# Optimization experiments

Measured on AMD Instinct MI355X. Metric: run time of the kernel, lower is better.

The kernel has to match this reference:

```python
import jax, jax.numpy as jnp
import numpy as np

L, S, N, E = 1024, 1024, 16, 1024

def setup_inputs() -> dict:
    key = jax.random.key(0)
    ks = jax.random.split(key, 7)
    return {
        "query": jax.random.normal(ks[0], (L, N, E), dtype=jnp.float32),
        "key": jax.random.normal(ks[1], (S, N, E), dtype=jnp.float32),
        "value": jax.random.normal(ks[2], (S, N, E), dtype=jnp.float32),
        "q_proj_weight": jax.random.normal(ks[3], (E, E), dtype=jnp.float32) * (E ** -0.5),
        "k_proj_weight": jax.random.normal(ks[4], (E, E), dtype=jnp.float32) * (E ** -0.5),
        "v_proj_weight": jax.random.normal(ks[5], (E, E), dtype=jnp.float32) * (E ** -0.5),
        "in_proj_bias": jax.random.normal(ks[6], (3 * E,), dtype=jnp.float32) * 0.02,
    }

def reference(query, key, value, q_proj_weight, k_proj_weight, v_proj_weight, in_proj_bias):
    # query: (L, N, E); key/value: (S, N, E); single head => head_dim = E
    e = query.shape[-1]
    scaling = jnp.asarray(e, query.dtype) ** -0.5
    # F.linear(x, W, b) = x @ W.T + b
    q = (jnp.einsum("lne,fe->lnf", query, q_proj_weight) + in_proj_bias[:e]) * scaling
    k = jnp.einsum("sne,fe->snf", key, k_proj_weight) + in_proj_bias[e:2 * e]
    v = jnp.einsum("sne,fe->snf", value, v_proj_weight) + in_proj_bias[2 * e:]
    # scores: (N, L, S)
    scores = jnp.einsum("lne,sne->nls", q, k)
    attn = jax.nn.softmax(scores, axis=-1)
    # output back to (L, N, E)
    out = jnp.einsum("nls,sne->lne", attn, v)
    return out
```

## Files before the change

kernel.cpp:

```cpp
#include <hip/hip_runtime.h>
#include <stdint.h>


typedef __attribute__((ext_vector_type(8))) short bf16x8;
typedef __attribute__((ext_vector_type(4))) float f32x4;

__device__ __forceinline__ float bf2f(unsigned short u) {
    union { unsigned int i; float f; } w; w.i = ((unsigned int)u) << 16; return w.f;
}
__device__ __forceinline__ unsigned short f2bf(float f) {
    union { float f; unsigned int i; } w; w.f = f;
    unsigned int r = (w.i + 0x7FFFu + ((w.i >> 16) & 1u)) >> 16;
    return (unsigned short)r;
}

__device__ __forceinline__ void g2l16(const unsigned short* g, unsigned short* l) {
    __builtin_amdgcn_global_load_lds(
        (const __attribute__((address_space(1))) unsigned int*)g,
        (__attribute__((address_space(3))) unsigned int*)l, 16, 0, 0);
}

#define BM 256
#define BN 256
#define BK 32

template <int BIAS_MODE, typename OutT>
__global__ __launch_bounds__(1024, 4) void gemm_bt2(
    const unsigned short* __restrict__ A,
    const unsigned short* __restrict__ B,
    OutT* __restrict__ C,
    const float* __restrict__ bias,
    float scale, int K,
    long lda, long ldb, long ldc,
    long aBatch, long bBatch, long cBatch,
    int gridM, int gridN)
{
    __shared__ __align__(16) unsigned short lds[65536];

    const int tid  = threadIdx.x;
    const int wave = tid >> 6;
    const int lane = tid & 63;
    const int lr   = lane & 15;
    const int q4   = lane >> 4;
    const int wm   = wave >> 2;
    const int wn   = wave & 3;

    const int p    = blockIdx.x;
    const int l    = ((p & 7) << 5) + (p >> 3);
    const int bcol = l % gridN;
    const int t2   = l / gridN;
    const int brow = t2 % gridM;
    const int bz   = t2 / gridM;

    const long m0 = (long)brow * BM;
    const long n0 = (long)bcol * BN;
    A += (long)bz * aBatch;
    B += (long)bz * bBatch;
    C += (long)bz * cBatch;

    const int tswz  = tid ^ ((tid >> 3) & 7);
    const int srow  = tswz >> 2;
    const int skoff = (tswz & 3) * 8;
    const unsigned short* aS = A + (m0 + srow) * lda + skoff;
    const unsigned short* bS = B + (n0 + srow) * ldb + skoff;
    const int ldsW = wave * 512;

    const int myoff = (((lr << 2) | q4) ^ ((lr >> 1) & 7)) << 3;

    f32x4 acc[4][4];
    const f32x4 zero = {0.f, 0.f, 0.f, 0.f};
#pragma unroll
    for (int m = 0; m < 4; m++)
#pragma unroll
        for (int n = 0; n < 4; n++) acc[m][n] = zero;

    const int nkt = K / BK;

#pragma unroll
    for (int t = 0; t < 3; t++) {
        const long kb = (long)t * BK;
        unsigned short* base = &lds[t * 16384];
        g2l16(aS + kb, base + ldsW);
        g2l16(bS + kb, base + 8192 + ldsW);
    }
    asm volatile("s_waitcnt vmcnt(4)" ::: "memory");
    __builtin_amdgcn_sched_barrier(0);
    __builtin_amdgcn_s_barrier();

    for (int kt = 0; kt < nkt; kt++) {
        const int buf  = kt & 3;
        const int sbuf = (kt + 3) & 3;
        const int st   = (kt + 3 < nkt) ? kt + 3 : nkt - 1;
        const long kb  = (long)st * BK;
        const unsigned short* At = &lds[buf * 16384];
        const unsigned short* Bt = At + 8192;
        unsigned short* sb = &lds[sbuf * 16384];

        g2l16(aS + kb, sb + ldsW);
        g2l16(bS + kb, sb + 8192 + ldsW);

        bf16x8 af[4], bfr[4];
#pragma unroll
        for (int m = 0; m < 4; m++)
            af[m] = *(const bf16x8*)&At[(wm * 64 + m * 16) * 32 + myoff];
#pragma unroll
        for (int n = 0; n < 4; n++)
            bfr[n] = *(const bf16x8*)&Bt[(wn * 64 + n * 16) * 32 + myoff];

        __builtin_amdgcn_s_setprio(1);
#pragma unroll
        for (int m = 0; m < 4; m++)
#pragma unroll
            for (int n = 0; n < 4; n++)
                acc[m][n] = __builtin_amdgcn_mfma_f32_16x16x32_bf16(
                    af[m], bfr[n], acc[m][n], 0, 0, 0);
        __builtin_amdgcn_s_setprio(0);

        asm volatile("s_waitcnt vmcnt(4)" ::: "memory");
        __builtin_amdgcn_sched_barrier(0);
        __builtin_amdgcn_s_barrier();
    }

    asm volatile("s_waitcnt vmcnt(0)" ::: "memory");
    __syncthreads();

    if constexpr (sizeof(OutT) == 2) {
#pragma unroll
        for (int m = 0; m < 4; m++)
#pragma unroll
            for (int n = 0; n < 4; n++) {
                const int col = wn * 64 + n * 16 + lr;
#pragma unroll
                for (int r = 0; r < 4; r++) {
                    const int row = wm * 64 + m * 16 + q4 * 4 + r;
                    float v = acc[m][n][r];
                    if constexpr (BIAS_MODE == 1) v += bias[n0 + col];
                    if constexpr (BIAS_MODE == 2) v += bias[m0 + row];
                    v *= scale;
                    lds[row * 256 + (col ^ (((row >> 2) & 3) << 4))] = f2bf(v);
                }
            }
        __syncthreads();
#pragma unroll
        for (int i = 0; i < 8; i++) {
            const int g   = i * 1024 + tid;
            const int row = g >> 5;
            const int ch  = g & 31;
            bf16x8 v = *(const bf16x8*)&lds[row * 256 + ((ch * 8) ^ (((row >> 2) & 3) << 4))];
            *(bf16x8*)((unsigned short*)C + (m0 + row) * ldc + n0 + ch * 8) = v;
        }
    } else {
        float* fl = (float*)lds;
#pragma unroll
        for (int h = 0; h < 2; h++) {
            __syncthreads();
            if ((wm >> 1) == h) {
#pragma unroll
                for (int m = 0; m < 4; m++)
#pragma unroll
                    for (int n = 0; n < 4; n++) {
                        const int col = wn * 64 + n * 16 + lr;
#pragma unroll
                        for (int r = 0; r < 4; r++) {
                            const int rowh = (wm & 1) * 64 + m * 16 + q4 * 4 + r;
                            float v = acc[m][n][r];
                            if constexpr (BIAS_MODE == 1) v += bias[n0 + col];
                            if constexpr (BIAS_MODE == 2) v += bias[m0 + h * 128 + rowh];
                            v *= scale;
                            fl[rowh * 256 + (col ^ (((rowh >> 2) & 3) << 4))] = v;
                        }
                    }
            }
            __syncthreads();
#pragma unroll
            for (int i = 0; i < 8; i++) {
                const int g   = i * 1024 + tid;
                const int row = g >> 6;
                const int ch  = g & 63;
                float4 v = *(const float4*)&fl[row * 256 + ((ch * 4) ^ (((row >> 2) & 3) << 4))];
                *(float4*)((float*)C + (m0 + h * 128 + row) * ldc + n0 + ch * 4) = v;
            }
        }
    }
}

__global__ __launch_bounds__(256) void cvt_all(
    const float* __restrict__ q,  unsigned short* __restrict__ qb,
    const float* __restrict__ k,  unsigned short* __restrict__ kb,
    const float* __restrict__ wq, const float* __restrict__ wk,
    const float* __restrict__ wv, unsigned short* __restrict__ wb)
{
    const int b = blockIdx.x;
    const float* src;
    unsigned short* dst;
    long item;
    if (b < 8192)       { src = q; dst = qb; item = (long)b * 256 + threadIdx.x; }
    else if (b < 16384) { src = k; dst = kb; item = (long)(b - 8192) * 256 + threadIdx.x; }
    else {
        const int wsel = (b - 16384) >> 9;
        src = (wsel == 0) ? wq : ((wsel == 1) ? wk : wv);
        dst = wb + (long)wsel * 1048576;
        item = (long)((b - 16384) & 511) * 256 + threadIdx.x;
    }
    const float4* pp = (const float4*)(src + item * 8);
    float4 a = pp[0], c = pp[1];
    bf16x8 v;
    v[0] = (short)f2bf(a.x); v[1] = (short)f2bf(a.y);
    v[2] = (short)f2bf(a.z); v[3] = (short)f2bf(a.w);
    v[4] = (short)f2bf(c.x); v[5] = (short)f2bf(c.y);
    v[6] = (short)f2bf(c.z); v[7] = (short)f2bf(c.w);
    *(bf16x8*)(dst + item * 8) = v;
}

__global__ __launch_bounds__(256) void cvt_one(
    const float* __restrict__ in, unsigned short* __restrict__ out)
{
    const long item = (long)blockIdx.x * 256 + threadIdx.x;
    const float4* pp = (const float4*)(in + item * 8);
    float4 a = pp[0], c = pp[1];
    bf16x8 v;
    v[0] = (short)f2bf(a.x); v[1] = (short)f2bf(a.y);
    v[2] = (short)f2bf(a.z); v[3] = (short)f2bf(a.w);
    v[4] = (short)f2bf(c.x); v[5] = (short)f2bf(c.y);
    v[6] = (short)f2bf(c.z); v[7] = (short)f2bf(c.w);
    *(bf16x8*)(out + item * 8) = v;
}

__global__ __launch_bounds__(256) void softmax_wave(unsigned short* __restrict__ base)
{
    const int wave = threadIdx.x >> 6, lane = threadIdx.x & 63;
    unsigned short* p = base + ((long)blockIdx.x * 4 + wave) * 1024;

    bf16x8 v0 = *(const bf16x8*)(p + lane * 8);
    bf16x8 v1 = *(const bf16x8*)(p + 512 + lane * 8);
    float x[16];
#pragma unroll
    for (int i = 0; i < 8; i++) {
        x[i]     = fminf(fmaxf(bf2f((unsigned short)v0[i]), -1e30f), 1e30f);
        x[8 + i] = fminf(fmaxf(bf2f((unsigned short)v1[i]), -1e30f), 1e30f);
    }
    float m = x[0];
#pragma unroll
    for (int i = 1; i < 16; i++) m = fmaxf(m, x[i]);
#pragma unroll
    for (int o = 32; o > 0; o >>= 1) m = fmaxf(m, __shfl_xor(m, o));

    float e[16], s = 0.f;
#pragma unroll
    for (int i = 0; i < 16; i++) { e[i] = __expf(x[i] - m); s += e[i]; }
#pragma unroll
    for (int o = 32; o > 0; o >>= 1) s += __shfl_xor(s, o);
    const float inv = 1.0f / s;

    bf16x8 o0, o1;
#pragma unroll
    for (int i = 0; i < 8; i++) {
        o0[i] = (short)f2bf(e[i] * inv);
        o1[i] = (short)f2bf(e[8 + i] * inv);
    }
    *(bf16x8*)(p + lane * 8) = o0;
    *(bf16x8*)(p + 512 + lane * 8) = o1;
}

extern "C" void kernel_launch(void* const* d_in, const int* in_sizes, int n_in,
                              void* d_out, int out_size, void* d_ws, size_t ws_size,
                              hipStream_t stream) {
    const float* query = (const float*)d_in[0];
    const float* keyp  = (const float*)d_in[1];
    const float* valp  = (const float*)d_in[2];
    const float* wq    = (const float*)d_in[3];
    const float* wk    = (const float*)d_in[4];
    const float* wv    = (const float*)d_in[5];
    const float* bias  = (const float*)d_in[6];
    float* out = (float*)d_out;

    unsigned short* WSA = (unsigned short*)d_ws;
    unsigned short* WSB = WSA + 16777216;
    unsigned short* OC  = (unsigned short*)d_out;
    unsigned short* OD  = OC + 16777216;

    const dim3 cblk(256, 1, 1);
    const dim3 gblk(1024, 1, 1);

    cvt_all<<<17920, cblk, 0, stream>>>(query, WSA, keyp, WSB, wq, wk, wv, OD);
    gemm_bt2<1, unsigned short><<<256, gblk, 0, stream>>>(
        WSA, OD, OC, bias, 0.03125f, 1024,
        1024, 1024, 1024, 0, 0, 0, 64, 4);
    gemm_bt2<1, unsigned short><<<256, gblk, 0, stream>>>(
        WSB, OD + 1048576, WSA, bias + 1024, 1.0f, 1024,
        1024, 1024, 1024, 0, 0, 0, 64, 4);
    gemm_bt2<0, unsigned short><<<256, gblk, 0, stream>>>(
        OC, WSA, WSB, nullptr, 1.0f, 1024,
        16384, 16384, 1024, 1024, 1024, 1048576, 4, 4);
    softmax_wave<<<4096, cblk, 0, stream>>>(WSB);
    cvt_one<<<8192, cblk, 0, stream>>>(valp, OC);
    gemm_bt2<2, unsigned short><<<256, gblk, 0, stream>>>(
        OD + 2097152, OC, WSA, bias + 2048, 1.0f, 1024,
        1024, 16384, 1024, 0, 1024, 1048576, 4, 4);
    gemm_bt2<0, float><<<256, gblk, 0, stream>>>(
        WSB, WSA, out, nullptr, 1.0f, 1024,
        1024, 1024, 16384, 1048576, 1048576, 1024, 4, 4);
}
```

Measured before the change: 422.5 us.

## Fuse fp32-to-bf16 input conversion into projection GEMM loads

```diff
diff --git a/kernel.cpp b/kernel.cpp
--- a/kernel.cpp
+++ b/kernel.cpp
@@ -24,10 +24,20 @@
 #define BN 256
 #define BK 32
 
-template <int BIAS_MODE, typename OutT>
+#define CVT8(dst8, r0, r1)                                                     \
+    {                                                                          \
+        bf16x8 _v;                                                             \
+        _v[0] = (short)f2bf((r0).x); _v[1] = (short)f2bf((r0).y);              \
+        _v[2] = (short)f2bf((r0).z); _v[3] = (short)f2bf((r0).w);              \
+        _v[4] = (short)f2bf((r1).x); _v[5] = (short)f2bf((r1).y);              \
+        _v[6] = (short)f2bf((r1).z); _v[7] = (short)f2bf((r1).w);              \
+        *(bf16x8*)(dst8) = _v;                                                 \
+    }
+
+template <int BIAS_MODE, typename OutT, bool INF32>
 __global__ __launch_bounds__(1024, 4) void gemm_bt2(
-    const unsigned short* __restrict__ A,
-    const unsigned short* __restrict__ B,
+    const void* __restrict__ Av,
+    const void* __restrict__ Bv,
     OutT* __restrict__ C,
     const float* __restrict__ bias,
     float scale, int K,
@@ -54,16 +64,10 @@
 
     const long m0 = (long)brow * BM;
     const long n0 = (long)bcol * BN;
-    A += (long)bz * aBatch;
-    B += (long)bz * bBatch;
-    C += (long)bz * cBatch;
 
     const int tswz  = tid ^ ((tid >> 3) & 7);
     const int srow  = tswz >> 2;
     const int skoff = (tswz & 3) * 8;
-    const unsigned short* aS = A + (m0 + srow) * lda + skoff;
-    const unsigned short* bS = B + (n0 + srow) * ldb + skoff;
-    const int ldsW = wave * 512;
 
     const int myoff = (((lr << 2) | q4) ^ ((lr >> 1) & 7)) << 3;
 
@@ -76,52 +80,121 @@
 
     const int nkt = K / BK;
 
-#pragma unroll
-    for (int t = 0; t < 3; t++) {
-        const long kb = (long)t * BK;
-        unsigned short* base = &lds[t * 16384];
-        g2l16(aS + kb, base + ldsW);
-        g2l16(bS + kb, base + 8192 + ldsW);
-    }
-    asm volatile("s_waitcnt vmcnt(4)" ::: "memory");
-    __builtin_amdgcn_sched_barrier(0);
-    __builtin_amdgcn_s_barrier();
-
-    for (int kt = 0; kt < nkt; kt++) {
-        const int buf  = kt & 3;
-        const int sbuf = (kt + 3) & 3;
-        const int st   = (kt + 3 < nkt) ? kt + 3 : nkt - 1;
-        const long kb  = (long)st * BK;
-        const unsigned short* At = &lds[buf * 16384];
-        const unsigned short* Bt = At + 8192;
-        unsigned short* sb = &lds[sbuf * 16384];
-
-        g2l16(aS + kb, sb + ldsW);
-        g2l16(bS + kb, sb + 8192 + ldsW);
-
-        bf16x8 af[4], bfr[4];
-#pragma unroll
-        for (int m = 0; m < 4; m++)
-            af[m] = *(const bf16x8*)&At[(wm * 64 + m * 16) * 32 + myoff];
-#pragma unroll
-        for (int n = 0; n < 4; n++)
-            bfr[n] = *(const bf16x8*)&Bt[(wn * 64 + n * 16) * 32 + myoff];
-
-        __builtin_amdgcn_s_setprio(1);
-#pragma unroll
-        for (int m = 0; m < 4; m++)
-#pragma unroll
-            for (int n = 0; n < 4; n++)
-                acc[m][n] = __builtin_amdgcn_mfma_f32_16x16x32_bf16(
-                    af[m], bfr[n], acc[m][n], 0, 0, 0);
-        __builtin_amdgcn_s_setprio(0);
-
+    if constexpr (!INF32) {
+        const unsigned short* A = (const unsigned short*)Av + (long)bz * aBatch;
+        const unsigned short* B = (const unsigned short*)Bv + (long)bz * bBatch;
+        const unsigned short* aS = A + (m0 + srow) * lda + skoff;
+        const unsigned short* bS = B + (n0 + srow) * ldb + skoff;
+        const int ldsW = wave * 512;
+
+#pragma unroll
+        for (int t = 0; t < 3; t++) {
+            const long kb = (long)t * BK;
+            unsigned short* base = &lds[t * 16384];
+            g2l16(aS + kb, base + ldsW);
+            g2l16(bS + kb, base + 8192 + ldsW);
+        }
         asm volatile("s_waitcnt vmcnt(4)" ::: "memory");
         __builtin_amdgcn_sched_barrier(0);
         __builtin_amdgcn_s_barrier();
-    }
-
-    asm volatile("s_waitcnt vmcnt(0)" ::: "memory");
+
+        for (int kt = 0; kt < nkt; kt++) {
+            const int buf  = kt & 3;
+            const int sbuf = (kt + 3) & 3;
+            const int st   = (kt + 3 < nkt) ? kt + 3 : nkt - 1;
+            const long kb  = (long)st * BK;
+            const unsigned short* At = &lds[buf * 16384];
+            const unsigned short* Bt = At + 8192;
+            unsigned short* sb = &lds[sbuf * 16384];
+
+            g2l16(aS + kb, sb + ldsW);
+            g2l16(bS + kb, sb + 8192 + ldsW);
+
+            bf16x8 af[4], bfr[4];
+#pragma unroll
+            for (int m = 0; m < 4; m++)
+                af[m] = *(const bf16x8*)&At[(wm * 64 + m * 16) * 32 + myoff];
+#pragma unroll
+            for (int n = 0; n < 4; n++)
+                bfr[n] = *(const bf16x8*)&Bt[(wn * 64 + n * 16) * 32 + myoff];
+
+            __builtin_amdgcn_s_setprio(1);
+#pragma unroll
+            for (int m = 0; m < 4; m++)
+#pragma unroll
+                for (int n = 0; n < 4; n++)
+                    acc[m][n] = __builtin_amdgcn_mfma_f32_16x16x32_bf16(
+                        af[m], bfr[n], acc[m][n], 0, 0, 0);
+            __builtin_amdgcn_s_setprio(0);
+
+            asm volatile("s_waitcnt vmcnt(4)" ::: "memory");
+            __builtin_amdgcn_sched_barrier(0);
+            __builtin_amdgcn_s_barrier();
+        }
+        asm volatile("s_waitcnt vmcnt(0)" ::: "memory");
+    } else {
+        const float* A = (const float*)Av + (long)bz * aBatch;
+        const float* B = (const float*)Bv + (long)bz * bBatch;
+        const float* aF = A + (m0 + srow) * lda + skoff;
+        const float* bF = B + (n0 + srow) * ldb + skoff;
+
+        float4 sa0, sa1, sb0, sb1;
+        sa0 = ((const float4*)aF)[0]; sa1 = ((const float4*)aF)[1];
+        sb0 = ((const float4*)bF)[0]; sb1 = ((const float4*)bF)[1];
+        {
+            unsigned short* w = &lds[tid * 8];
+            CVT8(w, sa0, sa1);
+            CVT8(w + 8192, sb0, sb1);
+        }
+        if (nkt > 1) {
+            sa0 = ((const float4*)(aF + BK))[0]; sa1 = ((const float4*)(aF + BK))[1];
+            sb0 = ((const float4*)(bF + BK))[0]; sb1 = ((const float4*)(bF + BK))[1];
+        }
+        asm volatile("s_waitcnt lgkmcnt(0)" ::: "memory");
+        __builtin_amdgcn_sched_barrier(0);
+        __builtin_amdgcn_s_barrier();
+
+        for (int kt = 0; kt < nkt; kt++) {
+            const unsigned short* At = &lds[(kt & 1) * 16384];
+            const unsigned short* Bt = At + 8192;
+
+            bf16x8 af[4], bfr[4];
+#pragma unroll
+            for (int m = 0; m < 4; m++)
+                af[m] = *(const bf16x8*)&At[(wm * 64 + m * 16) * 32 + myoff];
+#pragma unroll
+            for (int n = 0; n < 4; n++)
+                bfr[n] = *(const bf16x8*)&Bt[(wn * 64 + n * 16) * 32 + myoff];
+
+            if (kt + 1 < nkt) {
+                unsigned short* w = &lds[((kt + 1) & 1) * 16384 + tid * 8];
+                CVT8(w, sa0, sa1);
+                CVT8(w + 8192, sb0, sb1);
+            }
+            if (kt + 2 < nkt) {
+                const float* pa = aF + (long)(kt + 2) * BK;
+                const float* pb = bF + (long)(kt + 2) * BK;
+                sa0 = ((const float4*)pa)[0]; sa1 = ((const float4*)pa)[1];
+                sb0 = ((const float4*)pb)[0]; sb1 = ((const float4*)pb)[1];
+            }
+
+            __builtin_amdgcn_s_setprio(1);
+#pragma unroll
+            for (int m = 0; m < 4; m++)
+#pragma unroll
+                for (int n = 0; n < 4; n++)
+                    acc[m][n] = __builtin_amdgcn_mfma_f32_16x16x32_bf16(
+                        af[m], bfr[n], acc[m][n], 0, 0, 0);
+            __builtin_amdgcn_s_setprio(0);
+
+            asm volatile("s_waitcnt lgkmcnt(0)" ::: "memory");
+            __builtin_amdgcn_sched_barrier(0);
+            __builtin_amdgcn_s_barrier();
+        }
+    }
+
+    C += (long)bz * cBatch;
+
     __syncthreads();
 
     if constexpr (sizeof(OutT) == 2) {
@@ -182,48 +255,6 @@
             }
         }
     }
-}
-
-__global__ __launch_bounds__(256) void cvt_all(
-    const float* __restrict__ q,  unsigned short* __restrict__ qb,
-    const float* __restrict__ k,  unsigned short* __restrict__ kb,
-    const float* __restrict__ wq, const float* __restrict__ wk,
-    const float* __restrict__ wv, unsigned short* __restrict__ wb)
-{
-    const int b = blockIdx.x;
-    const float* src;
-    unsigned short* dst;
-    long item;
-    if (b < 8192)       { src = q; dst = qb; item = (long)b * 256 + threadIdx.x; }
-    else if (b < 16384) { src = k; dst = kb; item = (long)(b - 8192) * 256 + threadIdx.x; }
-    else {
-        const int wsel = (b - 16384) >> 9;
-        src = (wsel == 0) ? wq : ((wsel == 1) ? wk : wv);
-        dst = wb + (long)wsel * 1048576;
-        item = (long)((b - 16384) & 511) * 256 + threadIdx.x;
-    }
-    const float4* pp = (const float4*)(src + item * 8);
-    float4 a = pp[0], c = pp[1];
-    bf16x8 v;
-    v[0] = (short)f2bf(a.x); v[1] = (short)f2bf(a.y);
-    v[2] = (short)f2bf(a.z); v[3] = (short)f2bf(a.w);
-    v[4] = (short)f2bf(c.x); v[5] = (short)f2bf(c.y);
-    v[6] = (short)f2bf(c.z); v[7] = (short)f2bf(c.w);
-    *(bf16x8*)(dst + item * 8) = v;
-}
-
-__global__ __launch_bounds__(256) void cvt_one(
-    const float* __restrict__ in, unsigned short* __restrict__ out)
-{
-    const long item = (long)blockIdx.x * 256 + threadIdx.x;
-    const float4* pp = (const float4*)(in + item * 8);
-    float4 a = pp[0], c = pp[1];
-    bf16x8 v;
-    v[0] = (short)f2bf(a.x); v[1] = (short)f2bf(a.y);
-    v[2] = (short)f2bf(a.z); v[3] = (short)f2bf(a.w);
-    v[4] = (short)f2bf(c.x); v[5] = (short)f2bf(c.y);
-    v[6] = (short)f2bf(c.z); v[7] = (short)f2bf(c.w);
-    *(bf16x8*)(out + item * 8) = v;
 }
 
 __global__ __launch_bounds__(256) void softmax_wave(unsigned short* __restrict__ base)
@@ -282,22 +313,20 @@
     const dim3 cblk(256, 1, 1);
     const dim3 gblk(1024, 1, 1);
 
-    cvt_all<<<17920, cblk, 0, stream>>>(query, WSA, keyp, WSB, wq, wk, wv, OD);
-    gemm_bt2<1, unsigned short><<<256, gblk, 0, stream>>>(
-        WSA, OD, OC, bias, 0.03125f, 1024,
+    gemm_bt2<1, unsigned short, true><<<256, gblk, 0, stream>>>(
+        query, wq, OC, bias, 0.03125f, 1024,
         1024, 1024, 1024, 0, 0, 0, 64, 4);
-    gemm_bt2<1, unsigned short><<<256, gblk, 0, stream>>>(
-        WSB, OD + 1048576, WSA, bias + 1024, 1.0f, 1024,
+    gemm_bt2<1, unsigned short, true><<<256, gblk, 0, stream>>>(
+        keyp, wk, OD, bias + 1024, 1.0f, 1024,
         1024, 1024, 1024, 0, 0, 0, 64, 4);
-    gemm_bt2<0, unsigned short><<<256, gblk, 0, stream>>>(
-        OC, WSA, WSB, nullptr, 1.0f, 1024,
+    gemm_bt2<0, unsigned short, false><<<256, gblk, 0, stream>>>(
+        OC, OD, WSB, nullptr, 1.0f, 1024,
         16384, 16384, 1024, 1024, 1024, 1048576, 4, 4);
     softmax_wave<<<4096, cblk, 0, stream>>>(WSB);
-    cvt_one<<<8192, cblk, 0, stream>>>(valp, OC);
-    gemm_bt2<2, unsigned short><<<256, gblk, 0, stream>>>(
-        OD + 2097152, OC, WSA, bias + 2048, 1.0f, 1024,
+    gemm_bt2<2, unsigned short, true><<<256, gblk, 0, stream>>>(
+        wv, valp, WSA, bias + 2048, 1.0f, 1024,
         1024, 16384, 1024, 0, 1024, 1048576, 4, 4);
-    gemm_bt2<0, float><<<256, gblk, 0, stream>>>(
+    gemm_bt2<0, float, false><<<256, gblk, 0, stream>>>(
         WSB, WSA, out, nullptr, 1.0f, 1024,
         1024, 1024, 16384, 1048576, 1048576, 1024, 4, 4);
 }
```

Result: slower. 748.5 us (+77.1%).
